# Optimization experiments

Measured on AMD Instinct MI355X. Metric: run time of the kernel, lower is better.

## Reference

```python
import jax, jax.numpy as jnp
import numpy as np

N_NODES = 50000
D_FEAT = 128
N_EDGES = 800000
C = 1.0  # curvature (init kwarg)
MIN_NORM = 1e-15
ARTANH_EPS = 1e-15


def logmap0(x, c):
    # PoincareBall.logmap0: x/(sqrt(c)||x||) * artanh(sqrt(c)||x||), with the
    # same clamping as the torch repo (norm clamped to MIN_NORM, artanh arg to 1-eps).
    sqrt_c = c ** 0.5
    x_norm = jnp.maximum(jnp.linalg.norm(x, axis=-1, keepdims=True), MIN_NORM)
    u = jnp.clip(sqrt_c * x_norm, -1.0 + ARTANH_EPS, 1.0 - ARTANH_EPS)
    return x * (jnp.arctanh(u) / (sqrt_c * x_norm))


def setup_inputs() -> dict:
    key = jax.random.key(0)
    k1, k2, k3, k4 = jax.random.split(key, 4)
    # scale into the Poincare ball (||x|| < 1/sqrt(c))
    x = jax.random.normal(k1, (N_NODES, D_FEAT), dtype=jnp.float32) * 1e-3
    adj_rows = jax.random.randint(k2, (N_EDGES,), 0, N_NODES, dtype=jnp.int32)
    adj_cols = jax.random.randint(k3, (N_EDGES,), 0, N_NODES, dtype=jnp.int32)
    adj_vals = jax.random.uniform(k4, (N_EDGES,), dtype=jnp.float32)
    return {"x": x, "adj_rows": adj_rows, "adj_cols": adj_cols, "adj_vals": adj_vals}


def reference(x, adj_rows, adj_cols, adj_vals) -> jnp.ndarray:
    x_tangent = logmap0(x, C)                       # [N, d] elementwise hyperbolic map
    gathered = adj_vals[:, None] * x_tangent[adj_cols]  # [E, d] edge-parallel gather
    support_t = jax.ops.segment_sum(gathered, adj_rows, num_segments=N_NODES)  # [N, d]
    return support_t
```

## Files before the change

### kernel.cpp

```cpp
#include <hip/hip_runtime.h>
#include <math.h>

#define D_FEAT 128
#define NBINS 1024
#define BIN_MASK (NBINS - 1)
#define CAPB 1024
#define OCAP 4096
#define P1_EPB 6400

typedef float    v2f __attribute__((ext_vector_type(2)));
typedef int      v2i __attribute__((ext_vector_type(2)));
typedef float    v4f __attribute__((ext_vector_type(4)));
typedef unsigned v4u __attribute__((ext_vector_type(4)));

static __device__ inline unsigned short f2bf(float f) {
    unsigned u = __float_as_uint(f);
    u += 0x7FFFu + ((u >> 16) & 1u);
    return (unsigned short)(u >> 16);
}

__global__ void __launch_bounds__(256)
bin_scale_kernel(const float* __restrict__ x,
                 unsigned short* __restrict__ xt,
                 const int* __restrict__ rows,
                 const int* __restrict__ cols,
                 const float* __restrict__ vals,
                 int* __restrict__ gcur,
                 int* __restrict__ binned,
                 int* __restrict__ ocount,
                 int4* __restrict__ oedges,
                 int n_nodes, int n_edges, int n_scatter_blocks) {
    __shared__ int cnt1[NBINS];
    __shared__ int base1[NBINS];
    __shared__ int runc[NBINS];
    if ((int)blockIdx.x < n_scatter_blocks) {
        const int tid = threadIdx.x;
        for (int b = tid; b < NBINS; b += 256) { cnt1[b] = 0; runc[b] = 0; }
        __syncthreads();
        const int e0 = blockIdx.x * P1_EPB;
        const int e1 = min(e0 + P1_EPB, n_edges);
        for (int e = e0 + tid; e < e1; e += 256) {
            int r = __builtin_nontemporal_load(rows + e);
            atomicAdd(&cnt1[r & BIN_MASK], 1);
        }
        __syncthreads();
        for (int b = tid; b < NBINS; b += 256) {
            int c = cnt1[b];
            base1[b] = c ? atomicAdd(&gcur[b], c) : 0;
        }
        __syncthreads();
        for (int e = e0 + tid; e < e1; e += 256) {
            int   r = __builtin_nontemporal_load(rows + e);
            int   c = __builtin_nontemporal_load(cols + e);
            float v = __builtin_nontemporal_load(vals + e);
            int b = r & BIN_MASK;
            int slot = atomicAdd(&runc[b], 1);
            int idx = base1[b] + slot;
            if (idx < CAPB) {
                v2i p;
                p.x = c | ((r >> 10) << 16);
                p.y = __float_as_int(v);
                *((v2i*)(binned + 2 * ((size_t)b * CAPB + idx))) = p;
            } else {
                int o = atomicAdd(ocount, 1);
                if (o < OCAP) {
                    int4 q; q.x = r; q.y = c; q.z = __float_as_int(v); q.w = 0;
                    oedges[o] = q;
                }
            }
        }
    } else {
        const int lane = threadIdx.x & 63;
        const int wave = threadIdx.x >> 6;
        const int row = ((int)blockIdx.x - n_scatter_blocks) * 4 + wave;
        if (row >= n_nodes) return;

        v2f v = __builtin_nontemporal_load(
            (const v2f*)(x + (size_t)row * D_FEAT) + lane);
        float ss = v.x * v.x + v.y * v.y;
        #pragma unroll
        for (int off = 32; off > 0; off >>= 1)
            ss += __shfl_xor(ss, off, 64);

        float norm = sqrtf(ss);
        float nc = fmaxf(norm, 1e-15f);
        float u = fminf(nc, 1.0f - 1e-15f);
        float at = 0.5f * (log1pf(u) - log1pf(-u));
        float s = at / nc;

        unsigned packed = (unsigned)f2bf(v.x * s) |
                          ((unsigned)f2bf(v.y * s) << 16);
        __builtin_nontemporal_store(
            packed, (unsigned*)(xt + (size_t)row * D_FEAT) + lane);
    }
}

__global__ void __launch_bounds__(256)
gather_binned_kernel(const unsigned short* __restrict__ xt,
                     const int* __restrict__ gcur,
                     const int* __restrict__ binned,
                     const int* __restrict__ ocount,
                     const int4* __restrict__ oedges,
                     float* __restrict__ out, int n_nodes) {
    __shared__ v2i elist[CAPB];
    __shared__ v2i sorted[CAPB];
    __shared__ int rcnt[64], roff[64], rcur[64];

    const int bin = blockIdx.x;
    const int tid = threadIdx.x;
    const int total = gcur[bin];
    const bool over = total > CAPB;
    const int cnt = over ? CAPB : total;

    if (tid < 64) { rcnt[tid] = 0; rcur[tid] = 0; }
    __syncthreads();

    for (int i = tid; i < cnt; i += 256) {
        v2i w = ((const v2i*)(binned + 2 * (size_t)bin * CAPB))[i];
        elist[i] = w;
        atomicAdd(&rcnt[(w.x >> 16) & 63], 1);
    }
    __syncthreads();
    if (tid < 64) {
        int v = rcnt[tid];
        int s = v;
        #pragma unroll
        for (int off = 1; off < 64; off <<= 1) {
            int t = __shfl_up(s, off, 64);
            if (tid >= (unsigned)off) s += t;
        }
        roff[tid] = s - v;
    }
    __syncthreads();
    for (int i = tid; i < cnt; i += 256) {
        v2i w = elist[i];
        int l = (w.x >> 16) & 63;
        int slot = atomicAdd(&rcur[l], 1);
        sorted[roff[l] + slot] = w;
    }
    __syncthreads();

    const int lane = tid & 63;
    const int wave = tid >> 6;
    const int g = lane >> 4;
    const int t = lane & 15;

    for (int l = wave; l < 49; l += 4) {
        int row = bin + (l << 10);
        if (row >= n_nodes) break;
        int deg = rcnt[l];
        int off = roff[l];

        float a0 = 0, a1 = 0, a2 = 0, a3 = 0, a4 = 0, a5 = 0, a6 = 0, a7 = 0;

        for (int j = 0; j < deg; j += 8) {
            int i0 = j + g, i1 = j + 4 + g;
            v2i s0 = sorted[off + (i0 < deg ? i0 : 0)];
            v2i s1 = sorted[off + (i1 < deg ? i1 : 0)];
            float w0 = (i0 < deg) ? __int_as_float(s0.y) : 0.0f;
            float w1 = (i1 < deg) ? __int_as_float(s1.y) : 0.0f;
            int c0 = s0.x & 0xFFFF;
            int c1 = s1.x & 0xFFFF;
            v4u u0 = ((const v4u*)(xt + ((size_t)c0 << 7)))[t];
            v4u u1 = ((const v4u*)(xt + ((size_t)c1 << 7)))[t];
            a0 = fmaf(w0, __uint_as_float(u0.x << 16), a0);
            a1 = fmaf(w0, __uint_as_float(u0.x & 0xFFFF0000u), a1);
            a2 = fmaf(w0, __uint_as_float(u0.y << 16), a2);
            a3 = fmaf(w0, __uint_as_float(u0.y & 0xFFFF0000u), a3);
            a4 = fmaf(w0, __uint_as_float(u0.z << 16), a4);
            a5 = fmaf(w0, __uint_as_float(u0.z & 0xFFFF0000u), a5);
            a6 = fmaf(w0, __uint_as_float(u0.w << 16), a6);
            a7 = fmaf(w0, __uint_as_float(u0.w & 0xFFFF0000u), a7);
            a0 = fmaf(w1, __uint_as_float(u1.x << 16), a0);
            a1 = fmaf(w1, __uint_as_float(u1.x & 0xFFFF0000u), a1);
            a2 = fmaf(w1, __uint_as_float(u1.y << 16), a2);
            a3 = fmaf(w1, __uint_as_float(u1.y & 0xFFFF0000u), a3);
            a4 = fmaf(w1, __uint_as_float(u1.z << 16), a4);
            a5 = fmaf(w1, __uint_as_float(u1.z & 0xFFFF0000u), a5);
            a6 = fmaf(w1, __uint_as_float(u1.w << 16), a6);
            a7 = fmaf(w1, __uint_as_float(u1.w & 0xFFFF0000u), a7);
        }

        if (over) {
            int n = *ocount;
            n = n < OCAP ? n : OCAP;
            for (int j = 0; j < n; ++j) {
                int4 q = oedges[j];
                if (q.x == row) {
                    float w = (g == 0) ? __int_as_float(q.z) : 0.0f;
                    v4u u = ((const v4u*)(xt + ((size_t)q.y << 7)))[t];
                    a0 = fmaf(w, __uint_as_float(u.x << 16), a0);
                    a1 = fmaf(w, __uint_as_float(u.x & 0xFFFF0000u), a1);
                    a2 = fmaf(w, __uint_as_float(u.y << 16), a2);
                    a3 = fmaf(w, __uint_as_float(u.y & 0xFFFF0000u), a3);
                    a4 = fmaf(w, __uint_as_float(u.z << 16), a4);
                    a5 = fmaf(w, __uint_as_float(u.z & 0xFFFF0000u), a5);
                    a6 = fmaf(w, __uint_as_float(u.w << 16), a6);
                    a7 = fmaf(w, __uint_as_float(u.w & 0xFFFF0000u), a7);
                }
            }
        }

        a0 += __shfl_xor(a0, 16, 64); a0 += __shfl_xor(a0, 32, 64);
        a1 += __shfl_xor(a1, 16, 64); a1 += __shfl_xor(a1, 32, 64);
        a2 += __shfl_xor(a2, 16, 64); a2 += __shfl_xor(a2, 32, 64);
        a3 += __shfl_xor(a3, 16, 64); a3 += __shfl_xor(a3, 32, 64);
        a4 += __shfl_xor(a4, 16, 64); a4 += __shfl_xor(a4, 32, 64);
        a5 += __shfl_xor(a5, 16, 64); a5 += __shfl_xor(a5, 32, 64);
        a6 += __shfl_xor(a6, 16, 64); a6 += __shfl_xor(a6, 32, 64);
        a7 += __shfl_xor(a7, 16, 64); a7 += __shfl_xor(a7, 32, 64);

        if (g == 0) {
            v4f* op = (v4f*)(out + ((size_t)row << 7) + t * 8);
            v4f o0; o0.x = a0; o0.y = a1; o0.z = a2; o0.w = a3;
            v4f o1; o1.x = a4; o1.y = a5; o1.z = a6; o1.w = a7;
            __builtin_nontemporal_store(o0, op);
            __builtin_nontemporal_store(o1, op + 1);
        }
    }
}

__global__ void fallback_kernel(const float* __restrict__ x,
                                const int* __restrict__ rows,
                                const int* __restrict__ cols,
                                const float* __restrict__ vals,
                                float* __restrict__ out, int n_edges) {
    int gid = blockIdx.x * blockDim.x + threadIdx.x;
    int e = gid >> 5, t = gid & 31;
    if (e >= n_edges) return;
    int c = cols[e];
    const float* xr = x + (size_t)c * D_FEAT;
    float ss = 0.0f;
    for (int i = 0; i < D_FEAT; ++i) ss += xr[i] * xr[i];
    float nc = fmaxf(sqrtf(ss), 1e-15f);
    float u = fminf(nc, 1.0f - 1e-15f);
    float w = vals[e] * (0.5f * (log1pf(u) - log1pf(-u))) / nc;
    const float4* xc = (const float4*)xr;
    float4 xv = xc[t];
    float* o = out + (size_t)rows[e] * D_FEAT + t * 4;
    atomicAdd(o + 0, w * xv.x);
    atomicAdd(o + 1, w * xv.y);
    atomicAdd(o + 2, w * xv.z);
    atomicAdd(o + 3, w * xv.w);
}


extern "C" void kernel_launch(void* const* d_in, const int* in_sizes, int n_in,
                              void* d_out, int out_size, void* d_ws, size_t ws_size,
                              hipStream_t stream) {
    const float* x    = (const float*)d_in[0];
    const int*   rows = (const int*)d_in[1];
    const int*   cols = (const int*)d_in[2];
    const float* vals = (const float*)d_in[3];
    float* out = (float*)d_out;

    const int n_nodes = in_sizes[0] / D_FEAT;
    const int n_edges = in_sizes[1];

    char* wsb = (char*)d_ws;
    const int n_scatter_blocks = (n_edges + P1_EPB - 1) / P1_EPB;
    const int n_scale_blocks   = (n_nodes + 3) / 4;

    size_t xt_bytes    = (size_t)n_nodes * D_FEAT * 2;
    size_t gcur_off    = xt_bytes;
    size_t ocount_off  = gcur_off + (size_t)NBINS * 4;
    size_t oedges_off  = (ocount_off + 4 + 255) & ~(size_t)255;
    size_t binned_off  = (oedges_off + (size_t)OCAP * 16 + 511) & ~(size_t)511;
    size_t need        = binned_off + (size_t)NBINS * CAPB * 8;

    if (ws_size >= need) {
        unsigned short* xt = (unsigned short*)wsb;
        int*  gcur    = (int*)(wsb + gcur_off);
        int*  ocount  = (int*)(wsb + ocount_off);
        int4* oedges  = (int4*)(wsb + oedges_off);
        int*  binned  = (int*)(wsb + binned_off);

        hipMemsetAsync(gcur, 0, ocount_off + 4 - gcur_off, stream);
        bin_scale_kernel<<<n_scatter_blocks + n_scale_blocks, 256, 0, stream>>>(
            x, xt, rows, cols, vals, gcur, binned, ocount, oedges,
            n_nodes, n_edges, n_scatter_blocks);
        gather_binned_kernel<<<NBINS, 256, 0, stream>>>(
            xt, gcur, binned, ocount, oedges, out, n_nodes);
    } else {
        hipMemsetAsync(out, 0, (size_t)out_size * sizeof(float), stream);
        long long total = (long long)n_edges * 32;
        fallback_kernel<<<(int)((total + 255) / 256), 256, 0, stream>>>(
            x, rows, cols, vals, out, n_edges);
    }
}
```

Baseline: 145.4 us.

## Double bin count, assign one 16-lane group per row, pad global bin counters

Doubles the number of bins to 2048 with a smaller per-bin capacity, so the gather kernel launches twice as many blocks, each covering about 25 rows. Each row is now handled by a single 16-lane group that walks its edges sequentially, replacing the four-way edge split per wave and removing the cross-group shuffle reduction. The global bin counters are spaced 32 ints apart to reduce atomic contention on shared cache lines, and launch bounds request higher occupancy. The risk is serialised per-row edge loops with less memory-level parallelism per row, and more overflow edges now that capacity per bin is halved.

```diff
diff --git a/kernel.cpp b/kernel.cpp
--- a/kernel.cpp
+++ b/kernel.cpp
@@ -2,11 +2,13 @@
 #include <math.h>
 
 #define D_FEAT 128
-#define NBINS 1024
+#define NBINS 2048
+#define BIN_SHIFT 11
 #define BIN_MASK (NBINS - 1)
-#define CAPB 1024
+#define CAPB 512
 #define OCAP 4096
 #define P1_EPB 6400
+#define GSTRIDE 32
 
 typedef float    v2f __attribute__((ext_vector_type(2)));
 typedef int      v2i __attribute__((ext_vector_type(2)));
@@ -46,7 +48,7 @@
         __syncthreads();
         for (int b = tid; b < NBINS; b += 256) {
             int c = cnt1[b];
-            base1[b] = c ? atomicAdd(&gcur[b], c) : 0;
+            base1[b] = c ? atomicAdd(&gcur[b * GSTRIDE], c) : 0;
         }
         __syncthreads();
         for (int e = e0 + tid; e < e1; e += 256) {
@@ -58,7 +60,7 @@
             int idx = base1[b] + slot;
             if (idx < CAPB) {
                 v2i p;
-                p.x = c | ((r >> 10) << 16);
+                p.x = c | ((r >> BIN_SHIFT) << 16);
                 p.y = __float_as_int(v);
                 *((v2i*)(binned + 2 * ((size_t)b * CAPB + idx))) = p;
             } else {
@@ -95,7 +97,7 @@
     }
 }
 
-__global__ void __launch_bounds__(256)
+__global__ void __launch_bounds__(256, 8)
 gather_binned_kernel(const unsigned short* __restrict__ xt,
                      const int* __restrict__ gcur,
                      const int* __restrict__ binned,
@@ -104,61 +106,59 @@
                      float* __restrict__ out, int n_nodes) {
     __shared__ v2i elist[CAPB];
     __shared__ v2i sorted[CAPB];
-    __shared__ int rcnt[64], roff[64], rcur[64];
+    __shared__ int rcnt[32], roff[32], rcur[32];
 
     const int bin = blockIdx.x;
     const int tid = threadIdx.x;
-    const int total = gcur[bin];
+    const int total = gcur[bin * GSTRIDE];
     const bool over = total > CAPB;
     const int cnt = over ? CAPB : total;
 
-    if (tid < 64) { rcnt[tid] = 0; rcur[tid] = 0; }
+    if (tid < 32) { rcnt[tid] = 0; rcur[tid] = 0; }
     __syncthreads();
 
     for (int i = tid; i < cnt; i += 256) {
         v2i w = ((const v2i*)(binned + 2 * (size_t)bin * CAPB))[i];
         elist[i] = w;
-        atomicAdd(&rcnt[(w.x >> 16) & 63], 1);
-    }
-    __syncthreads();
-    if (tid < 64) {
+        atomicAdd(&rcnt[(w.x >> 16) & 31], 1);
+    }
+    __syncthreads();
+    if (tid < 32) {
         int v = rcnt[tid];
         int s = v;
         #pragma unroll
-        for (int off = 1; off < 64; off <<= 1) {
-            int t = __shfl_up(s, off, 64);
-            if (tid >= (unsigned)off) s += t;
+        for (int off = 1; off < 32; off <<= 1) {
+            int t = __shfl_up(s, off, 32);
+            if ((tid & 31) >= (unsigned)off) s += t;
         }
         roff[tid] = s - v;
     }
     __syncthreads();
     for (int i = tid; i < cnt; i += 256) {
         v2i w = elist[i];
-        int l = (w.x >> 16) & 63;
+        int l = (w.x >> 16) & 31;
         int slot = atomicAdd(&rcur[l], 1);
         sorted[roff[l] + slot] = w;
     }
     __syncthreads();
 
-    const int lane = tid & 63;
-    const int wave = tid >> 6;
-    const int g = lane >> 4;
-    const int t = lane & 15;
-
-    for (int l = wave; l < 49; l += 4) {
-        int row = bin + (l << 10);
-        if (row >= n_nodes) break;
-        int deg = rcnt[l];
-        int off = roff[l];
+    const int grp = tid >> 4;
+    const int t   = tid & 15;
+    const int nrows = (n_nodes - bin + NBINS - 1) >> BIN_SHIFT;
+
+    for (int l = grp; l < nrows; l += 16) {
+        const int row = bin + (l << BIN_SHIFT);
+        const int deg = rcnt[l];
+        const int off = roff[l];
 
         float a0 = 0, a1 = 0, a2 = 0, a3 = 0, a4 = 0, a5 = 0, a6 = 0, a7 = 0;
 
-        for (int j = 0; j < deg; j += 8) {
-            int i0 = j + g, i1 = j + 4 + g;
-            v2i s0 = sorted[off + (i0 < deg ? i0 : 0)];
-            v2i s1 = sorted[off + (i1 < deg ? i1 : 0)];
-            float w0 = (i0 < deg) ? __int_as_float(s0.y) : 0.0f;
-            float w1 = (i1 < deg) ? __int_as_float(s1.y) : 0.0f;
+        for (int j = 0; j < deg; j += 2) {
+            v2i s0 = sorted[off + j];
+            bool h1 = (j + 1) < deg;
+            v2i s1 = sorted[off + (h1 ? j + 1 : j)];
+            float w0 = __int_as_float(s0.y);
+            float w1 = h1 ? __int_as_float(s1.y) : 0.0f;
             int c0 = s0.x & 0xFFFF;
             int c1 = s1.x & 0xFFFF;
             v4u u0 = ((const v4u*)(xt + ((size_t)c0 << 7)))[t];
@@ -187,7 +187,7 @@
             for (int j = 0; j < n; ++j) {
                 int4 q = oedges[j];
                 if (q.x == row) {
-                    float w = (g == 0) ? __int_as_float(q.z) : 0.0f;
+                    float w = __int_as_float(q.z);
                     v4u u = ((const v4u*)(xt + ((size_t)q.y << 7)))[t];
                     a0 = fmaf(w, __uint_as_float(u.x << 16), a0);
                     a1 = fmaf(w, __uint_as_float(u.x & 0xFFFF0000u), a1);
@@ -201,22 +201,11 @@
             }
         }
 
-        a0 += __shfl_xor(a0, 16, 64); a0 += __shfl_xor(a0, 32, 64);
-        a1 += __shfl_xor(a1, 16, 64); a1 += __shfl_xor(a1, 32, 64);
-        a2 += __shfl_xor(a2, 16, 64); a2 += __shfl_xor(a2, 32, 64);
-        a3 += __shfl_xor(a3, 16, 64); a3 += __shfl_xor(a3, 32, 64);
-        a4 += __shfl_xor(a4, 16, 64); a4 += __shfl_xor(a4, 32, 64);
-        a5 += __shfl_xor(a5, 16, 64); a5 += __shfl_xor(a5, 32, 64);
-        a6 += __shfl_xor(a6, 16, 64); a6 += __shfl_xor(a6, 32, 64);
-        a7 += __shfl_xor(a7, 16, 64); a7 += __shfl_xor(a7, 32, 64);
-
-        if (g == 0) {
-            v4f* op = (v4f*)(out + ((size_t)row << 7) + t * 8);
-            v4f o0; o0.x = a0; o0.y = a1; o0.z = a2; o0.w = a3;
-            v4f o1; o1.x = a4; o1.y = a5; o1.z = a6; o1.w = a7;
-            __builtin_nontemporal_store(o0, op);
-            __builtin_nontemporal_store(o1, op + 1);
-        }
+        v4f* op = (v4f*)(out + ((size_t)row << 7) + t * 8);
+        v4f o0; o0.x = a0; o0.y = a1; o0.z = a2; o0.w = a3;
+        v4f o1; o1.x = a4; o1.y = a5; o1.z = a6; o1.w = a7;
+        __builtin_nontemporal_store(o0, op);
+        __builtin_nontemporal_store(o1, op + 1);
     }
 }
 
@@ -263,7 +252,8 @@
 
     size_t xt_bytes    = (size_t)n_nodes * D_FEAT * 2;
     size_t gcur_off    = xt_bytes;
-    size_t ocount_off  = gcur_off + (size_t)NBINS * 4;
+    size_t gcur_bytes  = (size_t)NBINS * GSTRIDE * 4;
+    size_t ocount_off  = gcur_off + gcur_bytes;
     size_t oedges_off  = (ocount_off + 4 + 255) & ~(size_t)255;
     size_t binned_off  = (oedges_off + (size_t)OCAP * 16 + 511) & ~(size_t)511;
     size_t need        = binned_off + (size_t)NBINS * CAPB * 8;
```

After: 157.8 us. 8.5% more time.

## Assign one 16-lane group per row and double block size in binned gather

Applied to the files above, without the earlier changes.

The gather kernel now assigns each destination row to a 16-thread group instead of a whole 64-lane wave, with 32 groups per 512-thread block. Each group processes four edges per iteration serially and pads the sorted list with zero entries so the tail loads stay safe. This drops the cross-lane shuffle reduction and gives more rows in flight per block. The cost is that imbalance between rows of different degree stalls the lanes of a wave, plus extra register pressure from four outstanding row loads.

```diff
diff --git a/kernel.cpp b/kernel.cpp
--- a/kernel.cpp
+++ b/kernel.cpp
@@ -95,7 +95,7 @@
     }
 }
 
-__global__ void __launch_bounds__(256)
+__global__ void __launch_bounds__(512, 8)
 gather_binned_kernel(const unsigned short* __restrict__ xt,
                      const int* __restrict__ gcur,
                      const int* __restrict__ binned,
@@ -103,7 +103,7 @@
                      const int4* __restrict__ oedges,
                      float* __restrict__ out, int n_nodes) {
     __shared__ v2i elist[CAPB];
-    __shared__ v2i sorted[CAPB];
+    __shared__ v2i sorted[CAPB + 4];
     __shared__ int rcnt[64], roff[64], rcur[64];
 
     const int bin = blockIdx.x;
@@ -115,7 +115,7 @@
     if (tid < 64) { rcnt[tid] = 0; rcur[tid] = 0; }
     __syncthreads();
 
-    for (int i = tid; i < cnt; i += 256) {
+    for (int i = tid; i < cnt; i += 512) {
         v2i w = ((const v2i*)(binned + 2 * (size_t)bin * CAPB))[i];
         elist[i] = w;
         atomicAdd(&rcnt[(w.x >> 16) & 63], 1);
@@ -132,37 +132,43 @@
         roff[tid] = s - v;
     }
     __syncthreads();
-    for (int i = tid; i < cnt; i += 256) {
+    for (int i = tid; i < cnt; i += 512) {
         v2i w = elist[i];
         int l = (w.x >> 16) & 63;
         int slot = atomicAdd(&rcur[l], 1);
         sorted[roff[l] + slot] = w;
     }
+    if (tid < 4) { v2i z; z.x = 0; z.y = 0; sorted[cnt + tid] = z; }
     __syncthreads();
 
-    const int lane = tid & 63;
-    const int wave = tid >> 6;
-    const int g = lane >> 4;
-    const int t = lane & 15;
-
-    for (int l = wave; l < 49; l += 4) {
-        int row = bin + (l << 10);
-        if (row >= n_nodes) break;
-        int deg = rcnt[l];
-        int off = roff[l];
+    const int grp = tid >> 4;
+    const int t   = tid & 15;
+    const int nrows = (n_nodes - bin + NBINS - 1) >> 10;
+
+    for (int l = grp; l < nrows; l += 32) {
+        const int row = bin + (l << 10);
+        const int deg = rcnt[l];
+        const int off = roff[l];
 
         float a0 = 0, a1 = 0, a2 = 0, a3 = 0, a4 = 0, a5 = 0, a6 = 0, a7 = 0;
 
-        for (int j = 0; j < deg; j += 8) {
-            int i0 = j + g, i1 = j + 4 + g;
-            v2i s0 = sorted[off + (i0 < deg ? i0 : 0)];
-            v2i s1 = sorted[off + (i1 < deg ? i1 : 0)];
-            float w0 = (i0 < deg) ? __int_as_float(s0.y) : 0.0f;
-            float w1 = (i1 < deg) ? __int_as_float(s1.y) : 0.0f;
+        for (int j = 0; j < deg; j += 4) {
+            v2i s0 = sorted[off + j];
+            v2i s1 = sorted[off + j + 1];
+            v2i s2 = sorted[off + j + 2];
+            v2i s3 = sorted[off + j + 3];
+            float w0 = __int_as_float(s0.y);
+            float w1 = (j + 1 < deg) ? __int_as_float(s1.y) : 0.0f;
+            float w2 = (j + 2 < deg) ? __int_as_float(s2.y) : 0.0f;
+            float w3 = (j + 3 < deg) ? __int_as_float(s3.y) : 0.0f;
             int c0 = s0.x & 0xFFFF;
             int c1 = s1.x & 0xFFFF;
+            int c2 = s2.x & 0xFFFF;
+            int c3 = s3.x & 0xFFFF;
             v4u u0 = ((const v4u*)(xt + ((size_t)c0 << 7)))[t];
             v4u u1 = ((const v4u*)(xt + ((size_t)c1 << 7)))[t];
+            v4u u2 = ((const v4u*)(xt + ((size_t)c2 << 7)))[t];
+            v4u u3 = ((const v4u*)(xt + ((size_t)c3 << 7)))[t];
             a0 = fmaf(w0, __uint_as_float(u0.x << 16), a0);
             a1 = fmaf(w0, __uint_as_float(u0.x & 0xFFFF0000u), a1);
             a2 = fmaf(w0, __uint_as_float(u0.y << 16), a2);
@@ -179,6 +185,22 @@
             a5 = fmaf(w1, __uint_as_float(u1.z & 0xFFFF0000u), a5);
             a6 = fmaf(w1, __uint_as_float(u1.w << 16), a6);
             a7 = fmaf(w1, __uint_as_float(u1.w & 0xFFFF0000u), a7);
+            a0 = fmaf(w2, __uint_as_float(u2.x << 16), a0);
+            a1 = fmaf(w2, __uint_as_float(u2.x & 0xFFFF0000u), a1);
+            a2 = fmaf(w2, __uint_as_float(u2.y << 16), a2);
+            a3 = fmaf(w2, __uint_as_float(u2.y & 0xFFFF0000u), a3);
+            a4 = fmaf(w2, __uint_as_float(u2.z << 16), a4);
+            a5 = fmaf(w2, __uint_as_float(u2.z & 0xFFFF0000u), a5);
+            a6 = fmaf(w2, __uint_as_float(u2.w << 16), a6);
+            a7 = fmaf(w2, __uint_as_float(u2.w & 0xFFFF0000u), a7);
+            a0 = fmaf(w3, __uint_as_float(u3.x << 16), a0);
+            a1 = fmaf(w3, __uint_as_float(u3.x & 0xFFFF0000u), a1);
+            a2 = fmaf(w3, __uint_as_float(u3.y << 16), a2);
+            a3 = fmaf(w3, __uint_as_float(u3.y & 0xFFFF0000u), a3);
+            a4 = fmaf(w3, __uint_as_float(u3.z << 16), a4);
+            a5 = fmaf(w3, __uint_as_float(u3.z & 0xFFFF0000u), a5);
+            a6 = fmaf(w3, __uint_as_float(u3.w << 16), a6);
+            a7 = fmaf(w3, __uint_as_float(u3.w & 0xFFFF0000u), a7);
         }
 
         if (over) {
@@ -187,7 +209,7 @@
             for (int j = 0; j < n; ++j) {
                 int4 q = oedges[j];
                 if (q.x == row) {
-                    float w = (g == 0) ? __int_as_float(q.z) : 0.0f;
+                    float w = __int_as_float(q.z);
                     v4u u = ((const v4u*)(xt + ((size_t)q.y << 7)))[t];
                     a0 = fmaf(w, __uint_as_float(u.x << 16), a0);
                     a1 = fmaf(w, __uint_as_float(u.x & 0xFFFF0000u), a1);
@@ -201,22 +223,11 @@
             }
         }
 
-        a0 += __shfl_xor(a0, 16, 64); a0 += __shfl_xor(a0, 32, 64);
-        a1 += __shfl_xor(a1, 16, 64); a1 += __shfl_xor(a1, 32, 64);
-        a2 += __shfl_xor(a2, 16, 64); a2 += __shfl_xor(a2, 32, 64);
-        a3 += __shfl_xor(a3, 16, 64); a3 += __shfl_xor(a3, 32, 64);
-        a4 += __shfl_xor(a4, 16, 64); a4 += __shfl_xor(a4, 32, 64);
-        a5 += __shfl_xor(a5, 16, 64); a5 += __shfl_xor(a5, 32, 64);
-        a6 += __shfl_xor(a6, 16, 64); a6 += __shfl_xor(a6, 32, 64);
-        a7 += __shfl_xor(a7, 16, 64); a7 += __shfl_xor(a7, 32, 64);
-
-        if (g == 0) {
-            v4f* op = (v4f*)(out + ((size_t)row << 7) + t * 8);
-            v4f o0; o0.x = a0; o0.y = a1; o0.z = a2; o0.w = a3;
-            v4f o1; o1.x = a4; o1.y = a5; o1.z = a6; o1.w = a7;
-            __builtin_nontemporal_store(o0, op);
-            __builtin_nontemporal_store(o1, op + 1);
-        }
+        v4f* op = (v4f*)(out + ((size_t)row << 7) + t * 8);
+        v4f o0; o0.x = a0; o0.y = a1; o0.z = a2; o0.w = a3;
+        v4f o1; o1.x = a4; o1.y = a5; o1.z = a6; o1.w = a7;
+        __builtin_nontemporal_store(o0, op);
+        __builtin_nontemporal_store(o1, op + 1);
     }
 }
 
@@ -279,7 +290,7 @@
         bin_scale_kernel<<<n_scatter_blocks + n_scale_blocks, 256, 0, stream>>>(
             x, xt, rows, cols, vals, gcur, binned, ocount, oedges,
             n_nodes, n_edges, n_scatter_blocks);
-        gather_binned_kernel<<<NBINS, 256, 0, stream>>>(
+        gather_binned_kernel<<<NBINS, 512, 0, stream>>>(
             xt, gcur, binned, ocount, oedges, out, n_nodes);
     } else {
         hipMemsetAsync(out, 0, (size_t)out_size * sizeof(float), stream);
```

Result: slower. 152.9 us (+5.2%).
